# Kernel optimization log

Measured on AMD Instinct MI355X. Metric: run time of the kernel, lower is better.

## Reference

```python
import jax, jax.numpy as jnp
import numpy as np

EMBED_DIM = 1024
HID = EMBED_DIM // 2
N = 32768
L2_REG = 0.001
BN_EPS = 1e-5


def setup_inputs() -> dict:
    key = jax.random.key(0)
    ks = jax.random.split(key, 8)
    inp = {
        "item_emb": jax.random.normal(ks[0], (N, EMBED_DIM), jnp.float32),
        "pos_item_emb": jax.random.normal(ks[1], (N, EMBED_DIM), jnp.float32),
        "neg_item_emb": jax.random.normal(ks[2], (N, EMBED_DIM), jnp.float32),
        # Linear 1: embed_dim -> embed_dim/2 (xavier_normal init, zero bias)
        "W1": jax.random.normal(ks[3], (HID, EMBED_DIM), jnp.float32) * np.sqrt(2.0 / (EMBED_DIM + HID)),
        "b1": jnp.zeros((HID,), jnp.float32),
        # BatchNorm1d params / running stats (eval-mode semantics)
        "gamma": jnp.ones((HID,), jnp.float32),
        "beta": jnp.zeros((HID,), jnp.float32),
        "run_mean": jnp.zeros((HID,), jnp.float32),
        "run_var": jnp.ones((HID,), jnp.float32),
        # Linear 2: embed_dim/2 -> embed_dim
        "W2": jax.random.normal(ks[4], (EMBED_DIM, HID), jnp.float32) * np.sqrt(2.0 / (EMBED_DIM + HID)),
        "b2": jnp.zeros((EMBED_DIM,), jnp.float32),
    }
    return inp


def _net(x, W1, b1, gamma, beta, run_mean, run_var, W2, b2):
    # Linear -> BatchNorm1d (eval stats) -> LeakyReLU(0.1) -> (Dropout=identity) -> Linear
    h = x @ W1.T + b1                                   # [N, HID]
    h = (h - run_mean) * jax.lax.rsqrt(run_var + BN_EPS) * gamma + beta
    h = jnp.where(h >= 0, h, 0.1 * h)
    return h @ W2.T + b2                                # [N, EMBED_DIM]


def reference(item_emb, pos_item_emb, neg_item_emb,
              W1, b1, gamma, beta, run_mean, run_var, W2, b2):
    net = lambda x: _net(x, W1, b1, gamma, beta, run_mean, run_var, W2, b2)
    anchor_e = net(item_emb)
    pos_e = net(pos_item_emb)
    neg_e = net(neg_item_emb)

    dist_pos = jnp.linalg.norm(anchor_e - pos_e, axis=1)  # [N]
    dist_neg = jnp.linalg.norm(anchor_e - neg_e, axis=1)  # [N]

    # fused replacement of the per-sample python loop
    margins = jnp.where(dist_neg < dist_pos, dist_pos - dist_neg, 0.0)
    margin = jnp.quantile(margins, 0.25)  # Q1, linear interpolation (matches torch)

    loss_triplet = jax.nn.relu(dist_neg ** 2 - dist_pos ** 2 + margin)
    l2 = L2_REG * (jnp.sum(anchor_e ** 2) + jnp.sum(pos_e ** 2) + jnp.sum(neg_e ** 2)) / anchor_e.shape[0]
    return jnp.mean(loss_triplet + l2)
```

## Files before the change

kernel.cpp:

```cpp
#include <hip/hip_runtime.h>

#define NROWS 32768
#define DIM   1024
#define HIDD  512
#define M3    (3*NROWS)

using bf16x8 = __attribute__((ext_vector_type(8))) short;
using f32x4  = __attribute__((ext_vector_type(4))) float;

#define MFMA16(a,b,c) __builtin_amdgcn_mfma_f32_16x16x32_bf16(a,b,c,0,0,0)
#define WAIT_VM(N)  asm volatile("s_waitcnt vmcnt(" #N ")" ::: "memory")
#define WAIT_LGKM0  asm volatile("s_waitcnt lgkmcnt(0)" ::: "memory")
#define MEMFENCE    asm volatile("" ::: "memory")
#define BAR()       __builtin_amdgcn_s_barrier()
#define SCHEDB()    __builtin_amdgcn_sched_barrier(0)
#define SP1()       __builtin_amdgcn_s_setprio(1)
#define SP0()       __builtin_amdgcn_s_setprio(0)

static __device__ __forceinline__ unsigned cvtpk(float a, float b) {
    unsigned r;
    asm("v_cvt_pk_bf16_f32 %0, %1, %2" : "=v"(r) : "v"(a), "v"(b));
    return r;
}
static __device__ __forceinline__ void gload16(const void* gsrc, void* ldst) {
    __builtin_amdgcn_global_load_lds(
        (const __attribute__((address_space(1))) unsigned int*)gsrc,
        (__attribute__((address_space(3))) unsigned int*)ldst,
        16, 0, 0);
}

__global__ __launch_bounds__(256)
void cvt_kernel(const float* __restrict__ src, unsigned short* __restrict__ dst, int n4)
{
    const int i = blockIdx.x * 256 + threadIdx.x;
    if (i < n4) {
        float4 v = reinterpret_cast<const float4*>(src)[i];
        uint2 o;
        o.x = cvtpk(v.x, v.y);
        o.y = cvtpk(v.z, v.w);
        reinterpret_cast<uint2*>(dst)[i] = o;
    }
}

__global__ __launch_bounds__(256)
void gemm1_mfma(const float* __restrict__ x0, const float* __restrict__ x1,
                const float* __restrict__ x2,
                const unsigned short* __restrict__ W1bf,
                const float* __restrict__ b1, const float* __restrict__ gamma,
                const float* __restrict__ beta, const float* __restrict__ rmean,
                const float* __restrict__ rvar,
                unsigned short* __restrict__ h)
{
    __shared__ char smem[32768];
    char* const Xb = smem;
    char* const Wb = smem + 16384;

    const int lin = blockIdx.x;
    const int wgid = (lin & 7) * 384 + (lin >> 3);
    const int cb = wgid & 3;
    const int rb = wgid >> 2;
    const int tid  = threadIdx.x;
    const int lane = tid & 63, w = tid >> 6;
    const int wr = w >> 1, wc = w & 1;
    const int row0 = rb * 128;
    const int s = row0 >> 15;
    const float* x = (s == 0) ? x0 : (s == 1 ? x1 : x2);
    const int rl0 = row0 & (NROWS - 1);
    const int col0 = cb * 128;
    const int l15 = lane & 15, lq = lane >> 4;

    f32x4 acc[4][4] = {};
    float4 aR[8];

    #pragma unroll
    for (int p = 0; p < 8; ++p) {
        const int f = p * 256 + tid;
        const int r = f >> 4, c4 = f & 15;
        aR[p] = *reinterpret_cast<const float4*>(&x[(size_t)(rl0 + r) * DIM + c4 * 4]);
    }

    for (int t = 0; t < 16; ++t) {
        const int k0 = t * 64;
        #pragma unroll
        for (int p = 0; p < 8; ++p) {
            const int f = p * 256 + tid;
            const int r = f >> 4, c4 = f & 15;
            const unsigned off = (unsigned)((r * 128 + c4 * 8) ^ ((r & 7) << 4));
            uint2 o; o.x = cvtpk(aR[p].x, aR[p].y); o.y = cvtpk(aR[p].z, aR[p].w);
            *reinterpret_cast<uint2*>(Xb + off) = o;
        }
        #pragma unroll
        for (int c = 0; c < 4; ++c) {
            const int f = c * 256 + tid;
            const int panel = f >> 9;
            const int cc = (f >> 2) & 127;
            const int chunk = (f & 3) ^ ((cc >> 1) & 3);
            gload16(&W1bf[(size_t)(col0 + cc) * DIM + k0 + panel * 32 + chunk * 8],
                    Wb + (size_t)f * 16);
        }
        __syncthreads();
        if (t < 15) {
            #pragma unroll
            for (int p = 0; p < 8; ++p) {
                const int f = p * 256 + tid;
                const int r = f >> 4, c4 = f & 15;
                aR[p] = *reinterpret_cast<const float4*>(
                    &x[(size_t)(rl0 + r) * DIM + k0 + 64 + c4 * 4]);
            }
        }
        bf16x8 wf[2][4], xf[2][4];
        #pragma unroll
        for (int kk = 0; kk < 2; ++kk) {
            #pragma unroll
            for (int cf = 0; cf < 4; ++cf) {
                const int colr = wc * 64 + cf * 16 + l15;
                const int slq = lq ^ ((colr >> 1) & 3);
                wf[kk][cf] = *reinterpret_cast<const bf16x8*>(Wb + kk * 8192 + colr * 64 + slq * 16);
            }
            #pragma unroll
            for (int rf = 0; rf < 4; ++rf) {
                const int row = wr * 64 + rf * 16 + l15;
                xf[kk][rf] = *reinterpret_cast<const bf16x8*>(
                    Xb + ((row * 128 + kk * 64 + lq * 16) ^ ((row & 7) << 4)));
            }
        }
        #pragma unroll
        for (int kk = 0; kk < 2; ++kk)
            #pragma unroll
            for (int cf = 0; cf < 4; ++cf)
                #pragma unroll
                for (int rf = 0; rf < 4; ++rf)
                    acc[cf][rf] = MFMA16(wf[kk][cf], xf[kk][rf], acc[cf][rf]);
        __syncthreads();
    }

    float2* const sAB = (float2*)smem;
    if (tid < 128) {
        const int c = col0 + tid;
        const float a = rsqrtf(rvar[c] + 1e-5f) * gamma[c];
        sAB[tid] = make_float2(a, (b1[c] - rmean[c]) * a + beta[c]);
    }
    __syncthreads();

    #pragma unroll
    for (int cf = 0; cf < 4; ++cf) {
        const int cbase = wc * 64 + cf * 16 + lq * 4;
        const float2 ab0 = sAB[cbase + 0];
        const float2 ab1 = sAB[cbase + 1];
        const float2 ab2 = sAB[cbase + 2];
        const float2 ab3 = sAB[cbase + 3];
        #pragma unroll
        for (int rf = 0; rf < 4; ++rf) {
            const int r = row0 + wr * 64 + rf * 16 + l15;
            float v0 = fmaf(acc[cf][rf][0], ab0.x, ab0.y);
            float v1 = fmaf(acc[cf][rf][1], ab1.x, ab1.y);
            float v2 = fmaf(acc[cf][rf][2], ab2.x, ab2.y);
            float v3 = fmaf(acc[cf][rf][3], ab3.x, ab3.y);
            v0 = (v0 >= 0.f) ? v0 : 0.1f * v0;
            v1 = (v1 >= 0.f) ? v1 : 0.1f * v1;
            v2 = (v2 >= 0.f) ? v2 : 0.1f * v2;
            v3 = (v3 >= 0.f) ? v3 : 0.1f * v3;
            uint2 o; o.x = cvtpk(v0, v1); o.y = cvtpk(v2, v3);
            *reinterpret_cast<uint2*>(&h[(size_t)r * HIDD + col0 + cbase]) = o;
        }
    }
}

__global__ __launch_bounds__(512, 1)
void gemm2_mfma(const unsigned short* __restrict__ h,
                const unsigned short* __restrict__ W2bf,
                const float* __restrict__ b2,
                float* __restrict__ pdp, float* __restrict__ pdn,
                float* __restrict__ pl2)
{
    __shared__ char smem[114688];
    char* const Ab = smem;
    char* const Bb = smem + 49152;

    const int lin = blockIdx.x;
    const int wgid = (lin & 7) * 256 + (lin >> 3);
    const int cb = wgid & 3;
    const int rb = wgid >> 2;
    const int tid  = threadIdx.x;
    const int lane = tid & 63, w = tid >> 6;
    const int wm = w >> 2, wn = w & 3;
    const int row0 = rb * 64;
    const int col0 = cb * 256;
    const int l15 = lane & 15, lq = lane >> 4;

    f32x4 acc[6][4] = {};

    auto issueA = [&](int k0, char* Adst) {
        #pragma unroll
        for (int i = 0; i < 3; ++i) {
            const int f = i * 512 + tid;
            const int mrow = f >> 3, c = f & 7;
            const int mf = mrow >> 4, rr = mrow & 15;
            const int ss = mf % 3, rf = mf / 3;
            gload16(&h[((size_t)ss * NROWS + row0 + rf * 16 + rr) * HIDD + k0 + ((c ^ (mrow & 7)) << 3)],
                    Adst + f * 16);
        }
    };
    auto issueB = [&](int k0, char* Bdst) {
        #pragma unroll
        for (int i = 0; i < 4; ++i) {
            const int f = i * 512 + tid;
            const int col = f >> 3, c = f & 7;
            gload16(&W2bf[(size_t)(col0 + col) * HIDD + k0 + ((c ^ (col & 7)) << 3)],
                    Bdst + f * 16);
        }
    };
    auto readA = [&](bf16x8 (&a)[3][2], int mh, char* Abase) {
        #pragma unroll
        for (int mm = 0; mm < 3; ++mm) {
            const int row = (wm * 6 + mh * 3 + mm) * 16 + l15;
            const int swz = (row & 7) << 4;
            #pragma unroll
            for (int ks = 0; ks < 2; ++ks)
                a[mm][ks] = *reinterpret_cast<const bf16x8*>(
                    Abase + ((row * 128 + ks * 64 + lq * 16) ^ swz));
        }
    };
    auto readB = [&](bf16x8 (&b)[2][2], int nh, char* Bbase) {
        #pragma unroll
        for (int nn = 0; nn < 2; ++nn) {
            const int col = wn * 64 + (nh * 2 + nn) * 16 + l15;
            const int swz = (col & 7) << 4;
            #pragma unroll
            for (int ks = 0; ks < 2; ++ks)
                b[nn][ks] = *reinterpret_cast<const bf16x8*>(
                    Bbase + ((col * 128 + ks * 64 + lq * 16) ^ swz));
        }
    };

    issueA(0, Ab);
    MEMFENCE;
    issueB(0, Bb);
    WAIT_VM(0);
    BAR();

    for (int t = 0; t < 8; ++t) {
        char* const Apt = Ab + (t & 1) * 24576;
        char* const Apn = Ab + ((t & 1) ^ 1) * 24576;
        char* const Bpt = Bb + (t & 1) * 32768;
        char* const Bpn = Bb + ((t & 1) ^ 1) * 32768;
        const int kn = ((t < 7) ? (t + 1) : 7) * 64;

        bf16x8 a[3][2], b[2][2], a2[3][2];
        readA(a, 0, Apt);
        readB(b, 0, Bpt);
        issueA(kn, Apn);
        MEMFENCE;
        issueB(kn, Bpn);
        BAR(); WAIT_LGKM0; SCHEDB(); SP1();
        #pragma unroll
        for (int mm = 0; mm < 3; ++mm)
            #pragma unroll
            for (int nn = 0; nn < 2; ++nn)
                #pragma unroll
                for (int ks = 0; ks < 2; ++ks)
                    acc[mm][nn] = MFMA16(a[mm][ks], b[nn][ks], acc[mm][nn]);
        SP0(); BAR();
        readB(b, 1, Bpt);
        BAR(); WAIT_LGKM0; SCHEDB(); SP1();
        #pragma unroll
        for (int mm = 0; mm < 3; ++mm)
            #pragma unroll
            for (int nn = 0; nn < 2; ++nn)
                #pragma unroll
                for (int ks = 0; ks < 2; ++ks)
                    acc[mm][2 + nn] = MFMA16(a[mm][ks], b[nn][ks], acc[mm][2 + nn]);
        SP0(); BAR();
        readA(a2, 1, Apt);
        BAR(); WAIT_LGKM0; SCHEDB(); SP1();
        #pragma unroll
        for (int mm = 0; mm < 3; ++mm)
            #pragma unroll
            for (int nn = 0; nn < 2; ++nn)
                #pragma unroll
                for (int ks = 0; ks < 2; ++ks)
                    acc[3 + mm][2 + nn] = MFMA16(a2[mm][ks], b[nn][ks], acc[3 + mm][2 + nn]);
        SP0(); BAR();
        readB(b, 0, Bpt);
        WAIT_VM(0);
        BAR(); WAIT_LGKM0; SCHEDB(); SP1();
        #pragma unroll
        for (int mm = 0; mm < 3; ++mm)
            #pragma unroll
            for (int nn = 0; nn < 2; ++nn)
                #pragma unroll
                for (int ks = 0; ks < 2; ++ks)
                    acc[3 + mm][nn] = MFMA16(a2[mm][ks], b[nn][ks], acc[3 + mm][nn]);
        SP0(); BAR();
    }

    float b2c[4];
    #pragma unroll
    for (int nf = 0; nf < 4; ++nf) b2c[nf] = b2[col0 + wn * 64 + nf * 16 + l15];
    float l2t = 0.f;
    #pragma unroll
    for (int mh = 0; mh < 2; ++mh) {
        const int rbase = row0 + (wm * 2 + mh) * 16 + lq * 4;
        #pragma unroll
        for (int i = 0; i < 4; ++i) {
            float dp = 0.f, dn = 0.f;
            #pragma unroll
            for (int nf = 0; nf < 4; ++nf) {
                const float ea = acc[mh * 3 + 0][nf][i] + b2c[nf];
                const float ep = acc[mh * 3 + 1][nf][i] + b2c[nf];
                const float en = acc[mh * 3 + 2][nf][i] + b2c[nf];
                dp += (ea - ep) * (ea - ep);
                dn += (ea - en) * (ea - en);
                l2t += ea * ea + ep * ep + en * en;
            }
            #pragma unroll
            for (int mm = 1; mm < 16; mm <<= 1) {
                dp += __shfl_xor(dp, mm);
                dn += __shfl_xor(dn, mm);
            }
            if (l15 == 0) {
                pdp[(size_t)(cb * 4 + wn) * NROWS + rbase + i] = dp;
                pdn[(size_t)(cb * 4 + wn) * NROWS + rbase + i] = dn;
            }
        }
    }
    #pragma unroll
    for (int mm = 1; mm < 64; mm <<= 1) l2t += __shfl_xor(l2t, mm);
    __syncthreads();
    float* const l2red = (float*)smem;
    if (lane == 0) l2red[w] = l2t;
    __syncthreads();
    if (tid == 0) {
        float t = 0.f;
        #pragma unroll
        for (int ww = 0; ww < 8; ++ww) t += l2red[ww];
        pl2[wgid] = t;
    }
}

__global__ __launch_bounds__(256)
void margins_kernel(const float* __restrict__ pdp, const float* __restrict__ pdn,
                    float* __restrict__ margins, float* __restrict__ dd)
{
    const int r = blockIdx.x * 256 + threadIdx.x;
    float dp2 = 0.f, dn2 = 0.f;
    #pragma unroll
    for (int q = 0; q < 16; ++q) {
        dp2 += pdp[(size_t)q * NROWS + r];
        dn2 += pdn[(size_t)q * NROWS + r];
    }
    dd[r] = dn2 - dp2;
    margins[r] = (dn2 < dp2) ? (sqrtf(dp2) - sqrtf(dn2)) : 0.f;
}

__global__ __launch_bounds__(1024)
void final_kernel(const float* __restrict__ pl2, int npl2,
                  const float* __restrict__ margins, const float* __restrict__ dd,
                  float* __restrict__ out)
{
    __shared__ unsigned hist[256];
    __shared__ float warp_red[16];
    __shared__ unsigned sh_prefix;
    __shared__ int sh_k;
    __shared__ float sh_l2;
    __shared__ unsigned sh_cle;
    __shared__ unsigned sh_minAbove;
    const int tid = threadIdx.x;

    float l2 = 0.f;
    for (int i = tid; i < npl2; i += 1024) l2 += pl2[i];
    #pragma unroll
    for (int m = 1; m < 64; m <<= 1) l2 += __shfl_xor(l2, m);
    if ((tid & 63) == 0) warp_red[tid >> 6] = l2;
    __syncthreads();
    if (tid == 0) {
        float t = 0.f;
        for (int w = 0; w < 16; ++w) t += warp_red[w];
        sh_l2 = t;
        sh_k = 8191; sh_prefix = 0u;
        sh_cle = 0u; sh_minAbove = 0xFFFFFFFFu;
    }
    __syncthreads();

    for (int shift = 24; shift >= 0; shift -= 8) {
        if (tid < 256) hist[tid] = 0u;
        __syncthreads();
        const unsigned prefix = sh_prefix;
        const unsigned mask = (shift == 24) ? 0u : (0xFFFFFFFFu << (shift + 8));
        for (int i = tid; i < NROWS; i += 1024) {
            const unsigned key = __float_as_uint(margins[i]);
            if (((key ^ prefix) & mask) == 0u)
                atomicAdd(&hist[(key >> shift) & 255u], 1u);
        }
        __syncthreads();
        if (tid == 0) {
            int kk = sh_k;
            unsigned cum = 0; int d = 0;
            for (; d < 256; ++d) {
                const unsigned c = hist[d];
                if (cum + c > (unsigned)kk) break;
                cum += c;
            }
            sh_prefix = prefix | ((unsigned)d << shift);
            sh_k = kk - (int)cum;
        }
        __syncthreads();
    }
    const unsigned p1u = sh_prefix;

    unsigned lc = 0, lmin = 0xFFFFFFFFu;
    for (int i = tid; i < NROWS; i += 1024) {
        const unsigned key = __float_as_uint(margins[i]);
        if (key <= p1u) ++lc; else lmin = min(lmin, key);
    }
    #pragma unroll
    for (int m = 1; m < 64; m <<= 1) {
        lc += __shfl_xor(lc, m);
        lmin = min(lmin, (unsigned)__shfl_xor((int)lmin, m));
    }
    if ((tid & 63) == 0) {
        atomicAdd(&sh_cle, lc);
        atomicMin(&sh_minAbove, lmin);
    }
    __syncthreads();
    const float p1 = __uint_as_float(p1u);
    const float p2 = (sh_cle >= 8193u) ? p1 : __uint_as_float(sh_minAbove);
    const float margin = p1 + 0.75f * (p2 - p1);

    float ssum = 0.f;
    for (int i = tid; i < NROWS; i += 1024) {
        const float t = dd[i] + margin;
        ssum += (t > 0.f) ? t : 0.f;
    }
    #pragma unroll
    for (int m = 1; m < 64; m <<= 1) ssum += __shfl_xor(ssum, m);
    if ((tid & 63) == 0) warp_red[tid >> 6] = ssum;
    __syncthreads();
    if (tid == 0) {
        float S = 0.f;
        for (int w = 0; w < 16; ++w) S += warp_red[w];
        out[0] = S / (float)NROWS + 1e-3f * sh_l2 / (float)NROWS;
    }
}

extern "C" void kernel_launch(void* const* d_in, const int* in_sizes, int n_in,
                              void* d_out, int out_size, void* d_ws, size_t ws_size,
                              hipStream_t stream) {
    (void)in_sizes; (void)n_in; (void)out_size; (void)ws_size;
    const float* item = (const float*)d_in[0];
    const float* pos  = (const float*)d_in[1];
    const float* neg  = (const float*)d_in[2];
    const float* W1   = (const float*)d_in[3];
    const float* b1   = (const float*)d_in[4];
    const float* gam  = (const float*)d_in[5];
    const float* bet  = (const float*)d_in[6];
    const float* rmu  = (const float*)d_in[7];
    const float* rvr  = (const float*)d_in[8];
    const float* W2   = (const float*)d_in[9];
    const float* b2   = (const float*)d_in[10];

    char* ws = (char*)d_ws;
    unsigned short* h = (unsigned short*)ws;
    size_t off = (size_t)M3 * HIDD * sizeof(unsigned short);
    unsigned short* W1bf = (unsigned short*)(ws + off); off += (size_t)HIDD * DIM * 2;
    unsigned short* W2bf = (unsigned short*)(ws + off); off += (size_t)DIM * HIDD * 2;
    float* pdp = (float*)(ws + off); off += (size_t)16 * NROWS * 4;
    float* pdn = (float*)(ws + off); off += (size_t)16 * NROWS * 4;
    float* pl2 = (float*)(ws + off); off += (size_t)2048 * 4;
    float* margins = (float*)(ws + off); off += (size_t)NROWS * 4;
    float* dd = (float*)(ws + off); off += (size_t)NROWS * 4;

    cvt_kernel<<<dim3((HIDD*DIM/4 + 255)/256), 256, 0, stream>>>(W1, W1bf, HIDD*DIM/4);
    cvt_kernel<<<dim3((DIM*HIDD/4 + 255)/256), 256, 0, stream>>>(W2, W2bf, DIM*HIDD/4);
    gemm1_mfma<<<dim3(3072), 256, 0, stream>>>(
        item, pos, neg, W1bf, b1, gam, bet, rmu, rvr, h);
    gemm2_mfma<<<dim3(2048), 512, 0, stream>>>(
        h, W2bf, b2, pdp, pdn, pl2);
    margins_kernel<<<dim3(NROWS/256), 256, 0, stream>>>(pdp, pdn, margins, dd);
    final_kernel<<<1, 1024, 0, stream>>>(pl2, 2048, margins, dd, (float*)d_out);
}
```

Before: 438.9 us.

## Double-buffer gemm1 X tile in LDS and load W1 fragments directly to registers

Restructures the gemm1 main loop so the X tile is double-buffered in LDS with two register prefetch stages (two tiles ahead), leaving one barrier per k-step instead of two. W1 bf16 fragments now go straight from global memory into registers one tile ahead, skipping the LDS staging and swizzle. MFMA sections are raised in wave priority. This is meant to overlap global loads with compute and cut barrier stalls, at the cost of more registers and uncoalesced per-lane W1 reads from global/L2.

```diff
diff --git a/kernel.cpp b/kernel.cpp
--- a/kernel.cpp
+++ b/kernel.cpp
@@ -52,8 +52,6 @@
                 unsigned short* __restrict__ h)
 {
     __shared__ char smem[32768];
-    char* const Xb = smem;
-    char* const Wb = smem + 16384;
 
     const int lin = blockIdx.x;
     const int wgid = (lin & 7) * 384 + (lin >> 3);
@@ -70,69 +68,85 @@
     const int l15 = lane & 15, lq = lane >> 4;
 
     f32x4 acc[4][4] = {};
-    float4 aR[8];
-
-    #pragma unroll
-    for (int p = 0; p < 8; ++p) {
-        const int f = p * 256 + tid;
-        const int r = f >> 4, c4 = f & 15;
-        aR[p] = *reinterpret_cast<const float4*>(&x[(size_t)(rl0 + r) * DIM + c4 * 4]);
-    }
-
-    for (int t = 0; t < 16; ++t) {
-        const int k0 = t * 64;
+    float4 aRa[8], aRb[8];
+    bf16x8 wfA[2][4], wfB[2][4];
+
+    const int ldr = tid >> 4, ldc = tid & 15;
+    const float* xsrc = &x[(size_t)(rl0 + ldr) * DIM + ldc * 4];
+    const unsigned short* wbase = &W1bf[(size_t)(col0 + wc * 64 + l15) * DIM + lq * 8];
+
+    auto loadX = [&](float4 (&aR)[8], int k0) {
+        #pragma unroll
+        for (int p = 0; p < 8; ++p)
+            aR[p] = *reinterpret_cast<const float4*>(xsrc + (size_t)(p * 16) * DIM + k0);
+    };
+    auto stageX = [&](float4 (&aR)[8], char* Xdst) {
         #pragma unroll
         for (int p = 0; p < 8; ++p) {
-            const int f = p * 256 + tid;
-            const int r = f >> 4, c4 = f & 15;
-            const unsigned off = (unsigned)((r * 128 + c4 * 8) ^ ((r & 7) << 4));
+            const int r = p * 16 + ldr;
+            const unsigned off = (unsigned)((r * 128 + ldc * 8) ^ ((r & 7) << 4));
             uint2 o; o.x = cvtpk(aR[p].x, aR[p].y); o.y = cvtpk(aR[p].z, aR[p].w);
-            *reinterpret_cast<uint2*>(Xb + off) = o;
-        }
-        #pragma unroll
-        for (int c = 0; c < 4; ++c) {
-            const int f = c * 256 + tid;
-            const int panel = f >> 9;
-            const int cc = (f >> 2) & 127;
-            const int chunk = (f & 3) ^ ((cc >> 1) & 3);
-            gload16(&W1bf[(size_t)(col0 + cc) * DIM + k0 + panel * 32 + chunk * 8],
-                    Wb + (size_t)f * 16);
-        }
-        __syncthreads();
-        if (t < 15) {
-            #pragma unroll
-            for (int p = 0; p < 8; ++p) {
-                const int f = p * 256 + tid;
-                const int r = f >> 4, c4 = f & 15;
-                aR[p] = *reinterpret_cast<const float4*>(
-                    &x[(size_t)(rl0 + r) * DIM + k0 + 64 + c4 * 4]);
-            }
-        }
-        bf16x8 wf[2][4], xf[2][4];
-        #pragma unroll
-        for (int kk = 0; kk < 2; ++kk) {
-            #pragma unroll
-            for (int cf = 0; cf < 4; ++cf) {
-                const int colr = wc * 64 + cf * 16 + l15;
-                const int slq = lq ^ ((colr >> 1) & 3);
-                wf[kk][cf] = *reinterpret_cast<const bf16x8*>(Wb + kk * 8192 + colr * 64 + slq * 16);
-            }
+            *reinterpret_cast<uint2*>(Xdst + off) = o;
+        }
+    };
+    auto loadW = [&](bf16x8 (&wf)[2][4], int k0) {
+        #pragma unroll
+        for (int kk = 0; kk < 2; ++kk)
+            #pragma unroll
+            for (int cf = 0; cf < 4; ++cf)
+                wf[kk][cf] = *reinterpret_cast<const bf16x8*>(
+                    wbase + (size_t)(cf * 16) * DIM + k0 + kk * 32);
+    };
+    auto readXf = [&](bf16x8 (&xf)[2][4], char* At) {
+        #pragma unroll
+        for (int kk = 0; kk < 2; ++kk)
             #pragma unroll
             for (int rf = 0; rf < 4; ++rf) {
                 const int row = wr * 64 + rf * 16 + l15;
                 xf[kk][rf] = *reinterpret_cast<const bf16x8*>(
-                    Xb + ((row * 128 + kk * 64 + lq * 16) ^ ((row & 7) << 4)));
+                    At + ((row * 128 + kk * 64 + lq * 16) ^ ((row & 7) << 4)));
             }
-        }
-        #pragma unroll
-        for (int kk = 0; kk < 2; ++kk)
-            #pragma unroll
-            for (int cf = 0; cf < 4; ++cf)
-                #pragma unroll
-                for (int rf = 0; rf < 4; ++rf)
-                    acc[cf][rf] = MFMA16(wf[kk][cf], xf[kk][rf], acc[cf][rf]);
-        __syncthreads();
-    }
+    };
+
+    loadX(aRa, 0);
+    loadX(aRb, 64);
+    loadW(wfA, 0);
+    stageX(aRa, smem);
+    WAIT_LGKM0;
+    BAR(); SCHEDB();
+
+    #define G1_TILE(T, WFC, WFN, ARS, ARL)                                         \
+        do {                                                                       \
+            char* const At = smem + ((T) & 1) * 16384;                             \
+            char* const An = smem + (((T) & 1) ^ 1) * 16384;                       \
+            const int kw = (((T) + 1 < 16) ? (T) + 1 : 15) * 64;                   \
+            const int kx = (((T) + 2 < 16) ? (T) + 2 : 15) * 64;                   \
+            loadW(WFN, kw);                                                        \
+            bf16x8 xf[2][4];                                                       \
+            readXf(xf, At);                                                        \
+            SP1();                                                                 \
+            _Pragma("unroll")                                                      \
+            for (int kk = 0; kk < 2; ++kk)                                         \
+                _Pragma("unroll")                                                  \
+                for (int cf = 0; cf < 4; ++cf)                                     \
+                    _Pragma("unroll")                                              \
+                    for (int rf = 0; rf < 4; ++rf)                                 \
+                        acc[cf][rf] = MFMA16(WFC[kk][cf], xf[kk][rf], acc[cf][rf]);\
+            SP0();                                                                 \
+            stageX(ARS, An);                                                       \
+            loadX(ARL, kx);                                                        \
+            WAIT_LGKM0;                                                            \
+            BAR(); SCHEDB();                                                       \
+        } while (0)
+
+    #pragma unroll 1
+    for (int t2 = 0; t2 < 8; ++t2) {
+        G1_TILE(2 * t2,     wfA, wfB, aRb, aRa);
+        G1_TILE(2 * t2 + 1, wfB, wfA, aRa, aRb);
+    }
+    #undef G1_TILE
+
+    __syncthreads();
 
     float2* const sAB = (float2*)smem;
     if (tid < 128) {
```

Result: slower. 505.5 us (+15.2%).

## Double-buffer GEMM1 tiles via direct global-to-LDS fp32 loads with convert-on-read

Applied to the files above, without the earlier changes.

Reworks the first GEMM's main loop to double-buffer X and W tiles in shared memory. The fp32 activations are copied straight into LDS with a swizzle and converted to bf16 when fragments are read, replacing the register staging and convert-on-store path. The next tile's loads are issued before the current MFMAs, leaving one barrier per iteration instead of two, and MFMA priority is raised. LDS use grows from 32KB to 96KB per block, which lowers occupancy and doubles the LDS read traffic for X.

```diff
diff --git a/kernel.cpp b/kernel.cpp
--- a/kernel.cpp
+++ b/kernel.cpp
@@ -51,9 +51,9 @@
                 const float* __restrict__ rvar,
                 unsigned short* __restrict__ h)
 {
-    __shared__ char smem[32768];
+    __shared__ char smem[98304];
     char* const Xb = smem;
-    char* const Wb = smem + 16384;
+    char* const Wb = smem + 65536;
 
     const int lin = blockIdx.x;
     const int wgid = (lin & 7) * 384 + (lin >> 3);
@@ -70,60 +70,67 @@
     const int l15 = lane & 15, lq = lane >> 4;
 
     f32x4 acc[4][4] = {};
-    float4 aR[8];
-
-    #pragma unroll
-    for (int p = 0; p < 8; ++p) {
-        const int f = p * 256 + tid;
-        const int r = f >> 4, c4 = f & 15;
-        aR[p] = *reinterpret_cast<const float4*>(&x[(size_t)(rl0 + r) * DIM + c4 * 4]);
-    }
-
-    for (int t = 0; t < 16; ++t) {
+
+    auto stageTile = [&](int t) {
+        char* const Xd = Xb + (t & 1) * 32768;
+        char* const Wd = Wb + (t & 1) * 16384;
         const int k0 = t * 64;
         #pragma unroll
         for (int p = 0; p < 8; ++p) {
             const int f = p * 256 + tid;
-            const int r = f >> 4, c4 = f & 15;
-            const unsigned off = (unsigned)((r * 128 + c4 * 8) ^ ((r & 7) << 4));
-            uint2 o; o.x = cvtpk(aR[p].x, aR[p].y); o.y = cvtpk(aR[p].z, aR[p].w);
-            *reinterpret_cast<uint2*>(Xb + off) = o;
-        }
-        #pragma unroll
-        for (int c = 0; c < 4; ++c) {
-            const int f = c * 256 + tid;
-            const int panel = f >> 9;
-            const int cc = (f >> 2) & 127;
+            const int r = f >> 4, c = f & 15;
+            gload16(&x[(size_t)(rl0 + r) * DIM + k0 + ((c ^ (r & 15)) << 2)], Xd + f * 16);
+        }
+        #pragma unroll
+        for (int p = 0; p < 4; ++p) {
+            const int f = p * 256 + tid;
+            const int panel = f >> 9, cc = (f >> 2) & 127;
             const int chunk = (f & 3) ^ ((cc >> 1) & 3);
-            gload16(&W1bf[(size_t)(col0 + cc) * DIM + k0 + panel * 32 + chunk * 8],
-                    Wb + (size_t)f * 16);
-        }
-        __syncthreads();
-        if (t < 15) {
-            #pragma unroll
-            for (int p = 0; p < 8; ++p) {
-                const int f = p * 256 + tid;
-                const int r = f >> 4, c4 = f & 15;
-                aR[p] = *reinterpret_cast<const float4*>(
-                    &x[(size_t)(rl0 + r) * DIM + k0 + 64 + c4 * 4]);
-            }
-        }
-        bf16x8 wf[2][4], xf[2][4];
-        #pragma unroll
-        for (int kk = 0; kk < 2; ++kk) {
+            gload16(&W1bf[(size_t)(col0 + cc) * DIM + k0 + panel * 32 + chunk * 8], Wd + f * 16);
+        }
+    };
+    auto readWf = [&](bf16x8 (&wf)[2][4], char* Wt) {
+        #pragma unroll
+        for (int kk = 0; kk < 2; ++kk)
             #pragma unroll
             for (int cf = 0; cf < 4; ++cf) {
                 const int colr = wc * 64 + cf * 16 + l15;
                 const int slq = lq ^ ((colr >> 1) & 3);
-                wf[kk][cf] = *reinterpret_cast<const bf16x8*>(Wb + kk * 8192 + colr * 64 + slq * 16);
-            }
+                wf[kk][cf] = *reinterpret_cast<const bf16x8*>(Wt + kk * 8192 + colr * 64 + slq * 16);
+            }
+    };
+    auto readXf = [&](bf16x8 (&xf)[2][4], char* Xt) {
+        #pragma unroll
+        for (int kk = 0; kk < 2; ++kk)
             #pragma unroll
             for (int rf = 0; rf < 4; ++rf) {
                 const int row = wr * 64 + rf * 16 + l15;
-                xf[kk][rf] = *reinterpret_cast<const bf16x8*>(
-                    Xb + ((row * 128 + kk * 64 + lq * 16) ^ ((row & 7) << 4)));
-            }
-        }
+                const int lc0 = kk * 8 + lq * 2;
+                const float4 u = *reinterpret_cast<const float4*>(
+                    Xt + row * 256 + ((lc0 ^ (row & 15)) << 4));
+                const float4 v = *reinterpret_cast<const float4*>(
+                    Xt + row * 256 + (((lc0 + 1) ^ (row & 15)) << 4));
+                uint4 q;
+                q.x = cvtpk(u.x, u.y); q.y = cvtpk(u.z, u.w);
+                q.z = cvtpk(v.x, v.y); q.w = cvtpk(v.z, v.w);
+                xf[kk][rf] = *reinterpret_cast<const bf16x8*>(&q);
+            }
+    };
+
+    stageTile(0);
+    WAIT_VM(0);
+    BAR(); SCHEDB();
+
+    #pragma unroll 1
+    for (int t = 0; t < 16; ++t) {
+        char* const Xt = Xb + (t & 1) * 32768;
+        char* const Wt = Wb + (t & 1) * 16384;
+        if (t < 15) stageTile(t + 1);
+        MEMFENCE;
+        bf16x8 wf[2][4], xf[2][4];
+        readWf(wf, Wt);
+        readXf(xf, Xt);
+        SP1();
         #pragma unroll
         for (int kk = 0; kk < 2; ++kk)
             #pragma unroll
@@ -131,8 +138,13 @@
                 #pragma unroll
                 for (int rf = 0; rf < 4; ++rf)
                     acc[cf][rf] = MFMA16(wf[kk][cf], xf[kk][rf], acc[cf][rf]);
-        __syncthreads();
-    }
+        SP0();
+        WAIT_VM(0);
+        WAIT_LGKM0;
+        BAR(); SCHEDB();
+    }
+
+    __syncthreads();
 
     float2* const sAB = (float2*)smem;
     if (tid < 128) {
```

New measurement: 550.6 us. 25.4% more time.
